# Optimization experiments

Hardware: AMD Instinct MI355X
Metric: run time of the kernel (lower is better)

## Reference

```python
import jax, jax.numpy as jnp
import numpy as np

B, T, N, C = 32, 16, 1000, 16   # batch, seq_len, num_nodes, in_channels
G, H, O = 32, 512, 8            # gcn_hidden, lstm_hidden, output_dim
E_RAND = 8000                   # random edges; + N self loops -> E = 9000


def setup_inputs() -> dict:
    key = jax.random.key(0)
    ks = jax.random.split(key, 13)
    rng = np.random.default_rng(0)
    src = rng.integers(0, N, E_RAND)
    dst = rng.integers(0, N, E_RAND)
    loop = np.arange(N)
    edge_index = jnp.asarray(
        np.stack([np.concatenate([src, loop]), np.concatenate([dst, loop])]),
        dtype=jnp.int32)
    ew = np.concatenate([rng.uniform(0.5, 1.5, E_RAND), np.ones(N)]).astype(np.float32)

    def p(k, s, sc):
        return jax.random.normal(k, s, jnp.float32) * sc

    return {
        'x': p(ks[0], (B, T, N, C), 1.0),
        'edge_index': edge_index,
        'edge_weight': jnp.asarray(ew),
        'gcn_w': p(ks[1], (T, C, G), 0.1),
        'gcn_b': p(ks[2], (T, G), 0.02),
        'w_ih0': p(ks[3], (4 * H, N * G), 0.02),
        'w_hh0': p(ks[4], (4 * H, H), 0.02),
        'b_ih0': p(ks[5], (4 * H,), 0.02),
        'b_hh0': p(ks[6], (4 * H,), 0.02),
        'w_ih1': p(ks[7], (4 * H, H), 0.02),
        'w_hh1': p(ks[8], (4 * H, H), 0.02),
        'b_ih1': p(ks[9], (4 * H,), 0.02),
        'b_hh1': p(ks[10], (4 * H,), 0.02),
        'proj_w': p(ks[11], (O, H), 0.04),
        'proj_b': p(ks[12], (O,), 0.02),
    }


def _lstm_layer(inp, w_ih, w_hh, b_ih, b_hh):
    # inp: [B, T, D]; torch gate order i, f, g, o
    pre = jnp.einsum('btd,gd->btg', inp, w_ih) + b_ih + b_hh  # [B, T, 4H]
    h0 = jnp.zeros((inp.shape[0], w_hh.shape[1]), inp.dtype)

    def step(carry, x_t):
        h, c = carry
        gates = x_t + h @ w_hh.T
        i, f, g, o = jnp.split(gates, 4, axis=-1)
        c = jax.nn.sigmoid(f) * c + jax.nn.sigmoid(i) * jnp.tanh(g)
        h = jax.nn.sigmoid(o) * jnp.tanh(c)
        return (h, c), h

    _, hs = jax.lax.scan(step, (h0, h0), pre.transpose(1, 0, 2))  # [T, B, H]
    return hs.transpose(1, 0, 2)


def reference(x, edge_index, edge_weight, gcn_w, gcn_b,
              w_ih0, w_hh0, b_ih0, b_hh0,
              w_ih1, w_hh1, b_ih1, b_hh1, proj_w, proj_b):
    src, dst = edge_index[0], edge_index[1]
    # GCN symmetric normalization (self-loops already present in edge list)
    deg = jax.ops.segment_sum(edge_weight, dst, num_segments=N)
    dinv = jnp.where(deg > 0, jax.lax.rsqrt(jnp.maximum(deg, 1e-12)), 0.0)
    norm = dinv[src] * edge_weight * dinv[dst]  # [E]
    # per-timestep linear transform: distinct GCN weight per t
    xw = jnp.einsum('btni,tio->btno', x, gcn_w)  # [B, T, N, G]
    # gather from source nodes, scale, scatter-add into targets
    msg = xw[:, :, src, :] * norm[None, None, :, None]      # [B, T, E, G]
    agg = jnp.zeros_like(xw).at[:, :, dst, :].add(msg)      # [B, T, N, G]
    h = jax.nn.relu(agg + gcn_b[None, :, None, :])
    seq = h.reshape(B, T, N * G)                            # [B, T, N*G]
    out1 = _lstm_layer(seq, w_ih0, w_hh0, b_ih0, b_hh0)
    out2 = _lstm_layer(out1, w_ih1, w_hh1, b_ih1, b_hh1)
    last = out2[:, -1, :]                                   # [B, H]
    return last @ proj_w.T + proj_b                         # [B, O]
```

## Files before the change

### kernel.cpp

```cpp
#include <hip/hip_runtime.h>
#include <hip/hip_bf16.h>

typedef unsigned short u16;
typedef __bf16 bf16x8 __attribute__((ext_vector_type(8)));
typedef float f32x4 __attribute__((ext_vector_type(4)));
typedef unsigned short u16x8 __attribute__((ext_vector_type(8)));
typedef unsigned long long u64;

#define NB 32
#define NT 16
#define NN 1000
#define NC 16
#define NG 32
#define NH 512
#define NK 32000
#define BH (NB*NH)
#define LWG 64
#define LTH 384
#define NSPLIT 8

__device__ __forceinline__ u16 f2bf(float f) {
    unsigned int u = __float_as_uint(f);
    unsigned int r = u + 0x7FFFu + ((u >> 16) & 1u);
    return (u16)(r >> 16);
}

__device__ __forceinline__ unsigned cvt2(float a, float b) {
    unsigned r;
    asm("v_cvt_pk_bf16_f32 %0, %1, %2" : "=v"(r) : "v"(a), "v"(b));
    return r;
}

__device__ __forceinline__ float sigmoidf(float x) { return 1.f / (1.f + __expf(-x)); }

__device__ __forceinline__ float dot4(float4 a, float4 b) {
    return a.x * b.x + a.y * b.y + a.z * b.z + a.w * b.w;
}

#define AT_LOAD(p)    __hip_atomic_load((p), __ATOMIC_RELAXED, __HIP_MEMORY_SCOPE_AGENT)
#define AT_STORE(p,v) __hip_atomic_store((p), (v), __ATOMIC_RELAXED, __HIP_MEMORY_SCOPE_AGENT)

#define GLOAD16(g, l) __builtin_amdgcn_global_load_lds( \
    (const __attribute__((address_space(1))) void*)(g),  \
    (__attribute__((address_space(3))) void*)(l), 16, 0, 0)

__global__ void graph_prep(const int* __restrict__ ei, const float* __restrict__ ew, int E,
                           int* __restrict__ rowptr, int* __restrict__ csr_src,
                           float* __restrict__ csr_nrm) {
    __shared__ float degs[NN];
    __shared__ float dinv[NN];
    __shared__ int cnt[NN];
    __shared__ int rp[NN + 1];
    __shared__ int wsum[16];
    int tid = threadIdx.x, lane = tid & 63, wid = tid >> 6;
    for (int n = tid; n < NN; n += 1024) { degs[n] = 0.f; cnt[n] = 0; }
    __syncthreads();
    for (int e = tid; e < E; e += 1024) {
        int d = ei[E + e];
        atomicAdd(&degs[d], ew[e]);
        atomicAdd(&cnt[d], 1);
    }
    __syncthreads();
    for (int n = tid; n < NN; n += 1024) {
        float d = degs[n];
        dinv[n] = d > 0.f ? rsqrtf(fmaxf(d, 1e-12f)) : 0.f;
    }
    int v = (tid < NN) ? cnt[tid] : 0;
    int inc = v;
#pragma unroll
    for (int d = 1; d < 64; d <<= 1) {
        int u = __shfl_up(inc, d, 64);
        if (lane >= d) inc += u;
    }
    if (lane == 63) wsum[wid] = inc;
    __syncthreads();
    if (tid == 0) {
        int a = 0;
#pragma unroll
        for (int i = 0; i < 16; ++i) { int t = wsum[i]; wsum[i] = a; a += t; }
    }
    __syncthreads();
    int excl = inc - v + wsum[wid];
    if (tid <= NN) { rp[tid] = excl; rowptr[tid] = excl; }
    if (tid < NN) cnt[tid] = 0;
    __syncthreads();
    for (int e = tid; e < E; e += 1024) {
        int d = ei[E + e], s = ei[e];
        int pos = rp[d] + atomicAdd(&cnt[d], 1);
        csr_src[pos] = s;
        csr_nrm[pos] = dinv[s] * ew[e] * dinv[d];
    }
}

__global__ __launch_bounds__(1024) void gcn_fused(const float* __restrict__ x,
                                                  const float* __restrict__ gw,
                                                  const float* __restrict__ gb,
                                                  const int* __restrict__ rowptr,
                                                  const int* __restrict__ csr_src,
                                                  const float* __restrict__ csr_nrm,
                                                  u16* __restrict__ seq) {
    __shared__ float xwlds[NN * NG];
    __shared__ float wlds[NC * NG];
    __shared__ int rplds[NN + 1];
    int bt = blockIdx.x;
    int t = bt & 15;
    int tid = threadIdx.x;
    int g = tid & 31, grp = tid >> 5;

    for (int i = tid; i < NC * NG; i += 1024) wlds[i] = gw[t * NC * NG + i];
    for (int i = tid; i <= NN; i += 1024) rplds[i] = rowptr[i];
    __syncthreads();

    const float* xbt = x + (size_t)bt * NN * NC;
    for (int r = grp; r < NN; r += 32) {
        const float4* xr = (const float4*)(xbt + r * NC);
        float4 a0 = xr[0], a1 = xr[1], a2 = xr[2], a3 = xr[3];
        float acc = a0.x * wlds[g]        + a0.y * wlds[32 + g]
                  + a0.z * wlds[64 + g]   + a0.w * wlds[96 + g]
                  + a1.x * wlds[128 + g]  + a1.y * wlds[160 + g]
                  + a1.z * wlds[192 + g]  + a1.w * wlds[224 + g]
                  + a2.x * wlds[256 + g]  + a2.y * wlds[288 + g]
                  + a2.z * wlds[320 + g]  + a2.w * wlds[352 + g]
                  + a3.x * wlds[384 + g]  + a3.y * wlds[416 + g]
                  + a3.z * wlds[448 + g]  + a3.w * wlds[480 + g];
        xwlds[r * NG + g] = acc;
    }
    __syncthreads();

    float bias = gb[t * NG + g];
    u16* seqbt = seq + (size_t)bt * NK;
    for (int n = grp; n < NN; n += 32) {
        int p0 = rplds[n], p1 = rplds[n + 1];
        float acc = 0.f;
        for (int p = p0; p < p1; ++p)
            acc += csr_nrm[p] * xwlds[csr_src[p] * NG + g];
        seqbt[n * NG + g] = f2bf(fmaxf(acc + bias, 0.f));
    }
}

__global__ __launch_bounds__(256) void gemm_f32b(const u16* __restrict__ A,
                                                 const float* __restrict__ Bw,
                                                 float* __restrict__ part) {
    __shared__ __align__(16) u16 As[2][128 * 64];
    __shared__ __align__(16) u16 Bs[2][128 * 64];
    int tid = threadIdx.x;
    int lane = tid & 63, wid = tid >> 6;
    int wr = wid >> 1, wc = wid & 1;
    int bid = blockIdx.x;
    int s = bid & 7;
    int idx = bid >> 3;
    int tm = (idx & 3) * 128, tn = (idx >> 2) * 128;
    int ks0 = s * 62 + (s < 4 ? s : 4);
    int ksn = (s < 4) ? 63 : 62;

    int srow = tid >> 3, sc = tid & 7;
    int sce = sc ^ (srow & 7);
    const u16* gaBase = A + (size_t)(tm + srow) * NK + (size_t)ks0 * 64 + sce * 8;
    int br = tid >> 3, bc = tid & 7;
    int bce = bc ^ (br & 7);
    const float* gbBase = Bw + (size_t)(tn + br) * NK + (size_t)ks0 * 64 + bce * 8;

    f32x4 acc[4][4];
#pragma unroll
    for (int i = 0; i < 4; ++i)
#pragma unroll
        for (int j = 0; j < 4; ++j) acc[i][j] = (f32x4){0.f, 0.f, 0.f, 0.f};

    int fr = lane & 15, kq = lane >> 4, fs = fr & 7;

    float4 bqA[8], bqB[8];

    auto issueA = [&](int kt, int buf) {
#pragma unroll
        for (int q = 0; q < 4; ++q)
            GLOAD16(gaBase + (size_t)kt * 64 + (size_t)q * 32 * NK,
                    &As[buf][0] + srow * 64 + sc * 8 + q * 32 * 64);
    };
    auto loadB = [&](int kt, float4* dst) {
        const float* g = gbBase + (size_t)kt * 64;
#pragma unroll
        for (int q = 0; q < 4; ++q) {
            dst[2 * q]     = *(const float4*)(g + (size_t)q * 32 * NK);
            dst[2 * q + 1] = *(const float4*)(g + (size_t)q * 32 * NK + 4);
        }
    };
    auto cvtB = [&](const float4* src, int buf) {
#pragma unroll
        for (int q = 0; q < 4; ++q) {
            uint4 w;
            w.x = cvt2(src[2 * q].x, src[2 * q].y);
            w.y = cvt2(src[2 * q].z, src[2 * q].w);
            w.z = cvt2(src[2 * q + 1].x, src[2 * q + 1].y);
            w.w = cvt2(src[2 * q + 1].z, src[2 * q + 1].w);
            *(uint4*)(&Bs[buf][0] + (br + q * 32) * 64 + bc * 8) = w;
        }
    };
    auto mfmaStep = [&](int buf) {
        const u16* Ap = &As[buf][0];
        const u16* Bp = &Bs[buf][0];
#pragma unroll
        for (int kk = 0; kk < 2; ++kk) {
            int c0 = ((kq + kk * 4) ^ fs) * 8;
            bf16x8 af[4], bv[4];
#pragma unroll
            for (int fm = 0; fm < 4; ++fm)
                af[fm] = *(const bf16x8*)(Ap + (wr * 64 + fm * 16 + fr) * 64 + c0);
#pragma unroll
            for (int fn = 0; fn < 4; ++fn)
                bv[fn] = *(const bf16x8*)(Bp + (wc * 64 + fn * 16 + fr) * 64 + c0);
#pragma unroll
            for (int fm = 0; fm < 4; ++fm)
#pragma unroll
                for (int fn = 0; fn < 4; ++fn)
                    acc[fm][fn] = __builtin_amdgcn_mfma_f32_16x16x32_bf16(af[fm], bv[fn], acc[fm][fn], 0, 0, 0);
        }
    };

    issueA(0, 0);
    loadB(0, bqA);
    loadB(ksn > 1 ? 1 : 0, bqB);
    cvtB(bqA, 0);
    asm volatile("s_waitcnt lgkmcnt(0)" ::: "memory");
    asm volatile("s_barrier" ::: "memory");

#define STEP(KS, P, CUR, NXT)                                                  \
    {                                                                          \
        int kA = (KS) + 1 < ksn ? (KS) + 1 : ksn - 1;                          \
        int kB = (KS) + 2 < ksn ? (KS) + 2 : ksn - 1;                          \
        issueA(kA, (P) ^ 1);                         \
        loadB(kB, NXT);                     \
        mfmaStep(P);                                                           \
        cvtB(CUR, (P) ^ 1);                    \
        asm volatile("s_waitcnt vmcnt(8) lgkmcnt(0)" ::: "memory");            \
        asm volatile("s_barrier" ::: "memory");                                \
    }

    int ks = 0;
    while (ks + 2 <= ksn) {
        STEP(ks, 0, bqB, bqA);
        STEP(ks + 1, 1, bqA, bqB);
        ks += 2;
    }
    if (ks < ksn) {
        STEP(ks, 0, bqB, bqA);
    }
#undef STEP

    int rq = lane >> 4;
    size_t base = (size_t)s * 512 * 2048;
#pragma unroll
    for (int fm = 0; fm < 4; ++fm)
#pragma unroll
        for (int fn = 0; fn < 4; ++fn)
#pragma unroll
            for (int rr = 0; rr < 4; ++rr) {
                int m = tm + wr * 64 + fm * 16 + rq * 4 + rr;
                int n = tn + wc * 64 + fn * 16 + (lane & 15);
                part[base + (size_t)m * 2048 + n] = acc[fm][fn][rr];
            }
}

__global__ __launch_bounds__(256) void reduce_bias_p(const float* __restrict__ part,
                                                     const float* __restrict__ b_ih0,
                                                     const float* __restrict__ b_hh0,
                                                     float* __restrict__ pre0p) {
    int s = blockIdx.y;
    int r = blockIdx.x * 64 + (threadIdx.x & 63);
    int bq = threadIdx.x >> 6;
    float bias = b_ih0[r] + b_hh0[r];
#pragma unroll
    for (int b8 = 0; b8 < 8; ++b8) {
        int b = bq * 8 + b8;
        float acc = bias;
#pragma unroll
        for (int sk = 0; sk < NSPLIT; ++sk)
            acc += part[(size_t)sk * 1048576 + (size_t)(b * 16 + s) * 2048 + r];
        pre0p[((size_t)s * 2048 + r) * 32 + b] = acc;
    }
}

__global__ __launch_bounds__(256) void wperm(const float* __restrict__ w_hh0,
                                             const float* __restrict__ w_ih1,
                                             const float* __restrict__ w_hh1,
                                             u16* __restrict__ Wbig) {
    int rt = blockIdx.x;
    int wg = blockIdx.y;
    int tid = threadIdx.x;
#pragma unroll
    for (int it = 0; it < 4; ++it) {
        int idx = it * 256 + tid;
        int kt = idx >> 6, lane = idx & 63;
        int p = rt * 16 + (lane & 15);
        int gate = (p & 31) >> 3;
        int col = wg * 8 + (p & 7);
        const float* src;
        if (p < 32)      src = w_hh0 + (size_t)(gate * NH + col) * NH;
        else if (p < 64) src = w_ih1 + (size_t)(gate * NH + col) * NH;
        else             src = w_hh1 + (size_t)(gate * NH + col) * NH;
        int k0 = kt * 32 + (lane >> 4) * 8;
        float4 v0 = *(const float4*)(src + k0);
        float4 v1 = *(const float4*)(src + k0 + 4);
        u16x8 o;
        o[0] = f2bf(v0.x); o[1] = f2bf(v0.y); o[2] = f2bf(v0.z); o[3] = f2bf(v0.w);
        o[4] = f2bf(v1.x); o[5] = f2bf(v1.y); o[6] = f2bf(v1.z); o[7] = f2bf(v1.w);
        *(u16x8*)(Wbig + (((size_t)wg * 6 + rt) * 16 + kt) * 512 + lane * 8) = o;
    }
}

__global__ void init2(u16* h0, u16* h1, int* flags) {
    int i = blockIdx.x * 256 + threadIdx.x;
    if (i < 2 * BH) { h0[i] = 0; h1[i] = 0; }
    if (i < 1024) flags[i] = 0;
}

__global__ __launch_bounds__(LTH) void lstm2(const u16* __restrict__ Wbig,
                                             const float* __restrict__ pre0p,
                                             const float* __restrict__ b_ih1,
                                             const float* __restrict__ b_hh1,
                                             u16* __restrict__ h0buf,
                                             u16* __restrict__ h1buf,
                                             float* __restrict__ h1f,
                                             int* __restrict__ flags) {
    __shared__ __align__(16) u16 hA0[32 * 520];
    __shared__ __align__(16) u16 hA1[32 * 520];
    __shared__ float G[96][33];
    __shared__ float cst[2][8][32];
    __shared__ u16 hst[2][8][32];
    int wg = blockIdx.x, tid = threadIdx.x;
    int wid = tid >> 6, lane = tid & 63;
    int grp = wid >> 1;

    bf16x8 af[16];
    const u16* wsrc = Wbig + (size_t)wg * 49152 + wid * 8192 + lane * 8;
#pragma unroll
    for (int kt = 0; kt < 16; ++kt) af[kt] = *(const bf16x8*)(wsrc + kt * 512);

    if (tid < 512) ((float*)cst)[tid] = 0.f;

    int uj = (tid >> 5) & 7, ub = tid & 31;
    int ucol = wg * 8 + uj;
    float bs0 = 0.f, bs1 = 0.f, bs2 = 0.f, bs3 = 0.f;
    if (tid < 256) {
        bs0 = b_ih1[ucol] + b_hh1[ucol];
        bs1 = b_ih1[NH + ucol] + b_hh1[NH + ucol];
        bs2 = b_ih1[2 * NH + ucol] + b_hh1[2 * NH + ucol];
        bs3 = b_ih1[3 * NH + ucol] + b_hh1[3 * NH + ucol];
    }
    __syncthreads();

    for (int s = 0; s <= 16; ++s) {
        for (int r = wid; r < 64; r += 6) {
            const u64* src = (r < 32)
                ? (const u64*)(h0buf + ((s & 1) ^ 1) * BH + r * 512)
                : (const u64*)(h1buf + (s & 1) * BH + (r - 32) * 512);
            u16* dst = (r < 32) ? (hA0 + r * 520) : (hA1 + (r - 32) * 520);
            u64 v0 = AT_LOAD(src + lane);
            u64 v1 = AT_LOAD(src + 64 + lane);
            *(u64*)(dst + lane * 4) = v0;
            *(u64*)(dst + 256 + lane * 4) = v1;
        }
        float up0 = 0.f, up1 = 0.f, up2 = 0.f, up3 = 0.f;
        if (tid < 256 && s < 16) {
            const float* pp = pre0p + (size_t)s * 2048 * 32 + ub;
            up0 = pp[(size_t)ucol * 32];
            up1 = pp[((size_t)NH + ucol) * 32];
            up2 = pp[((size_t)2 * NH + ucol) * 32];
            up3 = pp[((size_t)3 * NH + ucol) * 32];
        }
        __syncthreads();

        bool active = (grp == 0) ? (s < 16) : (s >= 1);
        if (active) {
            const u16* hA = (grp < 2) ? hA0 : hA1;
            const u16* hp = hA + (lane & 15) * 520 + (lane >> 4) * 8;
            f32x4 a0 = (f32x4){0.f, 0.f, 0.f, 0.f};
            f32x4 a1 = (f32x4){0.f, 0.f, 0.f, 0.f};
#pragma unroll
            for (int kt = 0; kt < 16; ++kt) {
                bf16x8 b0 = *(const bf16x8*)(hp + kt * 32);
                bf16x8 b1 = *(const bf16x8*)(hp + 16 * 520 + kt * 32);
                a0 = __builtin_amdgcn_mfma_f32_16x16x32_bf16(af[kt], b0, a0, 0, 0, 0);
                a1 = __builtin_amdgcn_mfma_f32_16x16x32_bf16(af[kt], b1, a1, 0, 0, 0);
            }
            int r0 = wid * 16 + (lane >> 4) * 4;
#pragma unroll
            for (int rr = 0; rr < 4; ++rr) {
                G[r0 + rr][lane & 15] = a0[rr];
                G[r0 + rr][16 + (lane & 15)] = a1[rr];
            }
        }
        __syncthreads();

        if (tid < 256) {
            if (s < 16) {
                float gi = G[uj][ub] + up0;
                float gf = G[8 + uj][ub] + up1;
                float gg = G[16 + uj][ub] + up2;
                float go = G[24 + uj][ub] + up3;
                float c = sigmoidf(gf) * cst[0][uj][ub] + sigmoidf(gi) * tanhf(gg);
                cst[0][uj][ub] = c;
                hst[0][uj][ub] = f2bf(sigmoidf(go) * tanhf(c));
            }
            if (s >= 1) {
                float gi = G[32 + uj][ub] + G[64 + uj][ub] + bs0;
                float gf = G[40 + uj][ub] + G[72 + uj][ub] + bs1;
                float gg = G[48 + uj][ub] + G[80 + uj][ub] + bs2;
                float go = G[56 + uj][ub] + G[88 + uj][ub] + bs3;
                float c = sigmoidf(gf) * cst[1][uj][ub] + sigmoidf(gi) * tanhf(gg);
                cst[1][uj][ub] = c;
                float hv = sigmoidf(go) * tanhf(c);
                hst[1][uj][ub] = f2bf(hv);
                if (s == 16) h1f[ub * NH + ucol] = hv;
            }
        }
        __syncthreads();

        if (s < 16) {
            if (wid == 0) {
                if (lane < 32) {
                    union { u16 a[8]; u64 q[2]; } v;
#pragma unroll
                    for (int j = 0; j < 8; ++j) v.a[j] = hst[0][j][lane];
                    u64* d = (u64*)(h0buf + (s & 1) * BH + lane * 512 + wg * 8);
                    AT_STORE(d, v.q[0]); AT_STORE(d + 1, v.q[1]);
                } else if (s >= 1) {
                    int b = lane - 32;
                    union { u16 a[8]; u64 q[2]; } v;
#pragma unroll
                    for (int j = 0; j < 8; ++j) v.a[j] = hst[1][j][b];
                    u64* d = (u64*)(h1buf + ((s - 1) & 1) * BH + b * 512 + wg * 8);
                    AT_STORE(d, v.q[0]); AT_STORE(d + 1, v.q[1]);
                }
                asm volatile("s_waitcnt vmcnt(0)" ::: "memory");
                if (lane == 0) AT_STORE(&flags[wg * 16], s + 1);
                int target = s + 1;
                for (;;) {
                    int v = AT_LOAD(&flags[lane * 16]);
                    if (__all(v >= target)) break;
                    __builtin_amdgcn_s_sleep(1);
                }
            }
            __syncthreads();
        }
    }
}

__global__ __launch_bounds__(1024) void proj_k(const float* __restrict__ h1f,
                                               const float* __restrict__ proj_w,
                                               const float* __restrict__ proj_b,
                                               float* __restrict__ out) {
    __shared__ float pj[32][8][4];
    int tid = threadIdx.x;
    int b = tid >> 5, o = (tid >> 2) & 7, kq = tid & 3;
    const float4* hp = (const float4*)(h1f + (size_t)b * NH + kq * 128);
    const float4* wp = (const float4*)(proj_w + (size_t)o * NH + kq * 128);
    float acc = 0.f;
#pragma unroll 8
    for (int k = 0; k < 32; ++k) acc += dot4(hp[k], wp[k]);
    pj[b][o][kq] = acc;
    __syncthreads();
    if (tid < 256) {
        int bb = tid >> 3, oo = tid & 7;
        out[bb * 8 + oo] = pj[bb][oo][0] + pj[bb][oo][1] + pj[bb][oo][2] + pj[bb][oo][3] + proj_b[oo];
    }
}

extern "C" void kernel_launch(void* const* d_in, const int* in_sizes, int n_in,
                              void* d_out, int out_size, void* d_ws, size_t ws_size,
                              hipStream_t stream) {
    const float* x      = (const float*)d_in[0];
    const int*   ei     = (const int*)d_in[1];
    const float* ew     = (const float*)d_in[2];
    const float* gcn_w  = (const float*)d_in[3];
    const float* gcn_b  = (const float*)d_in[4];
    const float* w_ih0  = (const float*)d_in[5];
    const float* w_hh0  = (const float*)d_in[6];
    const float* b_ih0  = (const float*)d_in[7];
    const float* b_hh0  = (const float*)d_in[8];
    const float* w_ih1  = (const float*)d_in[9];
    const float* w_hh1  = (const float*)d_in[10];
    const float* b_ih1  = (const float*)d_in[11];
    const float* b_hh1  = (const float*)d_in[12];
    const float* proj_w = (const float*)d_in[13];
    const float* proj_b = (const float*)d_in[14];
    int E = in_sizes[2];

    char* ws = (char*)d_ws;
    size_t off = 0;
    float* part   = (float*)(ws + off);
    u16* Wbig     = (u16*)part;        off += 50331648;
    u16* seq      = (u16*)(ws + off);  off += 32768000;
    float* pre0p  = (float*)(ws + off); off += 4194304;
    u16* h0buf    = (u16*)(ws + off);  off += 2 * BH * 2;
    u16* h1buf    = (u16*)(ws + off);  off += 2 * BH * 2;
    float* h1f    = (float*)(ws + off); off += BH * 4;
    int* flags    = (int*)(ws + off);  off += 4096;
    int* rowptr   = (int*)(ws + off);  off += 4096;
    int* csr_src  = (int*)(ws + off);  off += 36864;
    float* csr_nrm = (float*)(ws + off); off += 36864;
    (void)ws_size; (void)n_in; (void)out_size;

    graph_prep<<<1, 1024, 0, stream>>>(ei, ew, E, rowptr, csr_src, csr_nrm);
    gcn_fused<<<512, 1024, 0, stream>>>(x, gcn_w, gcn_b, rowptr, csr_src, csr_nrm, seq);
    gemm_f32b<<<512, 256, 0, stream>>>(seq, w_ih0, part);
    reduce_bias_p<<<dim3(32, 16), 256, 0, stream>>>(part, b_ih0, b_hh0, pre0p);
    wperm<<<dim3(6, 64), 256, 0, stream>>>(w_hh0, w_ih1, w_hh1, Wbig);
    init2<<<128, 256, 0, stream>>>(h0buf, h1buf, flags);

    lstm2<<<LWG, LTH, 0, stream>>>(Wbig, pre0p, b_ih1, b_hh1, h0buf, h1buf, h1f, flags);
    proj_k<<<1, 1024, 0, stream>>>(h1f, proj_w, proj_b, (float*)d_out);
}
```

Baseline: 444.0 us.

## Restructure split-K input GEMM to load A directly into registers with 512x64 tiles

The layer-0 input-projection GEMM now covers all 512 rows per block with an N-tile of 64 (8 waves of 64 rows each). The A operand (bf16 GCN output) is read from global memory straight into MFMA register fragments instead of being staged through LDS; only the fp32 weight tile is converted and put in shared memory. This halves the grid to 256 blocks of 512 threads and removes the A LDS traffic and its async copies. In exchange, each fp32 weight element is read from HBM only once, but the A loads are strided 16-byte accesses per lane with less coalescing, and there is less explicit vmcnt-based overlap.

```diff
diff --git a/kernel.cpp b/kernel.cpp
--- a/kernel.cpp
+++ b/kernel.cpp
@@ -138,27 +138,27 @@
     }
 }
 
-__global__ __launch_bounds__(256) void gemm_f32b(const u16* __restrict__ A,
-                                                 const float* __restrict__ Bw,
-                                                 float* __restrict__ part) {
-    __shared__ __align__(16) u16 As[2][128 * 64];
-    __shared__ __align__(16) u16 Bs[2][128 * 64];
+__global__ __launch_bounds__(512) void gemm_sk(const u16* __restrict__ A,
+                                               const float* __restrict__ Bw,
+                                               float* __restrict__ part) {
+    __shared__ __align__(16) u16 Bs[2][64 * 64];
     int tid = threadIdx.x;
-    int lane = tid & 63, wid = tid >> 6;
-    int wr = wid >> 1, wc = wid & 1;
+    int lane = tid & 63, w = tid >> 6;
     int bid = blockIdx.x;
     int s = bid & 7;
-    int idx = bid >> 3;
-    int tm = (idx & 3) * 128, tn = (idx >> 2) * 128;
+    int tn = (bid >> 3) * 64;
     int ks0 = s * 62 + (s < 4 ? s : 4);
     int ksn = (s < 4) ? 63 : 62;
-
-    int srow = tid >> 3, sc = tid & 7;
-    int sce = sc ^ (srow & 7);
-    const u16* gaBase = A + (size_t)(tm + srow) * NK + (size_t)ks0 * 64 + sce * 8;
+    int fr = lane & 15, kq = lane >> 4, fs = fr & 7;
+
+    const u16* aRow0 = A + (size_t)(w * 64 +  0 + fr) * NK + (size_t)ks0 * 64 + kq * 8;
+    const u16* aRow1 = A + (size_t)(w * 64 + 16 + fr) * NK + (size_t)ks0 * 64 + kq * 8;
+    const u16* aRow2 = A + (size_t)(w * 64 + 32 + fr) * NK + (size_t)ks0 * 64 + kq * 8;
+    const u16* aRow3 = A + (size_t)(w * 64 + 48 + fr) * NK + (size_t)ks0 * 64 + kq * 8;
+
     int br = tid >> 3, bc = tid & 7;
-    int bce = bc ^ (br & 7);
-    const float* gbBase = Bw + (size_t)(tn + br) * NK + (size_t)ks0 * 64 + bce * 8;
+    const float* gB = Bw + (size_t)(tn + br) * NK + (size_t)ks0 * 64 + bc * 8;
+    int bwr = br * 64 + (bc ^ (br & 7)) * 8;
 
     f32x4 acc[4][4];
 #pragma unroll
@@ -166,85 +166,74 @@
 #pragma unroll
         for (int j = 0; j < 4; ++j) acc[i][j] = (f32x4){0.f, 0.f, 0.f, 0.f};
 
-    int fr = lane & 15, kq = lane >> 4, fs = fr & 7;
-
-    float4 bqA[8], bqB[8];
-
-    auto issueA = [&](int kt, int buf) {
-#pragma unroll
-        for (int q = 0; q < 4; ++q)
-            GLOAD16(gaBase + (size_t)kt * 64 + (size_t)q * 32 * NK,
-                    &As[buf][0] + srow * 64 + sc * 8 + q * 32 * 64);
+    bf16x8 aA[8], aB[8];
+    float4 bA[2], bB[2];
+
+    auto loadA = [&](int ks, bf16x8* dst) {
+        size_t o = (size_t)ks * 64;
+        dst[0] = *(const bf16x8*)(aRow0 + o);      dst[1] = *(const bf16x8*)(aRow0 + o + 32);
+        dst[2] = *(const bf16x8*)(aRow1 + o);      dst[3] = *(const bf16x8*)(aRow1 + o + 32);
+        dst[4] = *(const bf16x8*)(aRow2 + o);      dst[5] = *(const bf16x8*)(aRow2 + o + 32);
+        dst[6] = *(const bf16x8*)(aRow3 + o);      dst[7] = *(const bf16x8*)(aRow3 + o + 32);
     };
-    auto loadB = [&](int kt, float4* dst) {
-        const float* g = gbBase + (size_t)kt * 64;
-#pragma unroll
-        for (int q = 0; q < 4; ++q) {
-            dst[2 * q]     = *(const float4*)(g + (size_t)q * 32 * NK);
-            dst[2 * q + 1] = *(const float4*)(g + (size_t)q * 32 * NK + 4);
+    auto loadBf = [&](int ks, float4* dst) {
+        const float* g = gB + (size_t)ks * 64;
+        dst[0] = *(const float4*)g;
+        dst[1] = *(const float4*)(g + 4);
+    };
+    auto cvtWriteB = [&](const float4* src, int p) {
+        uint4 v;
+        v.x = cvt2(src[0].x, src[0].y); v.y = cvt2(src[0].z, src[0].w);
+        v.z = cvt2(src[1].x, src[1].y); v.w = cvt2(src[1].z, src[1].w);
+        *(uint4*)(&Bs[p][0] + bwr) = v;
+    };
+    auto mfmaStep = [&](const bf16x8* ar, int p) {
+#pragma unroll
+        for (int kk = 0; kk < 2; ++kk) {
+            bf16x8 bv[4];
+#pragma unroll
+            for (int fn = 0; fn < 4; ++fn) {
+                int row = fn * 16 + fr;
+                int chunk = (kq + kk * 4) ^ fs;
+                bv[fn] = *(const bf16x8*)(&Bs[p][0] + row * 64 + chunk * 8);
+            }
+#pragma unroll
+            for (int fm = 0; fm < 4; ++fm)
+#pragma unroll
+                for (int fn = 0; fn < 4; ++fn)
+                    acc[fm][fn] = __builtin_amdgcn_mfma_f32_16x16x32_bf16(ar[fm * 2 + kk], bv[fn], acc[fm][fn], 0, 0, 0);
         }
     };
-    auto cvtB = [&](const float4* src, int buf) {
-#pragma unroll
-        for (int q = 0; q < 4; ++q) {
-            uint4 w;
-            w.x = cvt2(src[2 * q].x, src[2 * q].y);
-            w.y = cvt2(src[2 * q].z, src[2 * q].w);
-            w.z = cvt2(src[2 * q + 1].x, src[2 * q + 1].y);
-            w.w = cvt2(src[2 * q + 1].z, src[2 * q + 1].w);
-            *(uint4*)(&Bs[buf][0] + (br + q * 32) * 64 + bc * 8) = w;
-        }
-    };
-    auto mfmaStep = [&](int buf) {
-        const u16* Ap = &As[buf][0];
-        const u16* Bp = &Bs[buf][0];
-#pragma unroll
-        for (int kk = 0; kk < 2; ++kk) {
-            int c0 = ((kq + kk * 4) ^ fs) * 8;
-            bf16x8 af[4], bv[4];
-#pragma unroll
-            for (int fm = 0; fm < 4; ++fm)
-                af[fm] = *(const bf16x8*)(Ap + (wr * 64 + fm * 16 + fr) * 64 + c0);
-#pragma unroll
-            for (int fn = 0; fn < 4; ++fn)
-                bv[fn] = *(const bf16x8*)(Bp + (wc * 64 + fn * 16 + fr) * 64 + c0);
-#pragma unroll
-            for (int fm = 0; fm < 4; ++fm)
-#pragma unroll
-                for (int fn = 0; fn < 4; ++fn)
-                    acc[fm][fn] = __builtin_amdgcn_mfma_f32_16x16x32_bf16(af[fm], bv[fn], acc[fm][fn], 0, 0, 0);
-        }
-    };
-
-    issueA(0, 0);
-    loadB(0, bqA);
-    loadB(ksn > 1 ? 1 : 0, bqB);
-    cvtB(bqA, 0);
+
+    loadA(0, aA);
+    loadBf(0, bA);
+    loadBf(ksn > 1 ? 1 : 0, bB);
+    cvtWriteB(bA, 0);
     asm volatile("s_waitcnt lgkmcnt(0)" ::: "memory");
     asm volatile("s_barrier" ::: "memory");
 
-#define STEP(KS, P, CUR, NXT)                                                  \
+#define GSTEP(KS, P, CA, NA, CB, NB_)                                          \
     {                                                                          \
         int kA = (KS) + 1 < ksn ? (KS) + 1 : ksn - 1;                          \
         int kB = (KS) + 2 < ksn ? (KS) + 2 : ksn - 1;                          \
-        issueA(kA, (P) ^ 1);                         \
-        loadB(kB, NXT);                     \
-        mfmaStep(P);                                                           \
-        cvtB(CUR, (P) ^ 1);                    \
-        asm volatile("s_waitcnt vmcnt(8) lgkmcnt(0)" ::: "memory");            \
+        loadA(kA, NA);                                                         \
+        loadBf(kB, NB_);                                                       \
+        mfmaStep(CA, P);                                                       \
+        cvtWriteB(CB, (P) ^ 1);                                                \
+        asm volatile("s_waitcnt lgkmcnt(0)" ::: "memory");                     \
         asm volatile("s_barrier" ::: "memory");                                \
     }
 
     int ks = 0;
     while (ks + 2 <= ksn) {
-        STEP(ks, 0, bqB, bqA);
-        STEP(ks + 1, 1, bqA, bqB);
+        GSTEP(ks, 0, aA, aB, bB, bA);
+        GSTEP(ks + 1, 1, aB, aA, bA, bB);
         ks += 2;
     }
     if (ks < ksn) {
-        STEP(ks, 0, bqB, bqA);
-    }
-#undef STEP
+        GSTEP(ks, 0, aA, aB, bB, bA);
+    }
+#undef GSTEP
 
     int rq = lane >> 4;
     size_t base = (size_t)s * 512 * 2048;
@@ -254,8 +243,8 @@
         for (int fn = 0; fn < 4; ++fn)
 #pragma unroll
             for (int rr = 0; rr < 4; ++rr) {
-                int m = tm + wr * 64 + fm * 16 + rq * 4 + rr;
-                int n = tn + wc * 64 + fn * 16 + (lane & 15);
+                int m = w * 64 + fm * 16 + rq * 4 + rr;
+                int n = tn + fn * 16 + (lane & 15);
                 part[base + (size_t)m * 2048 + n] = acc[fm][fn][rr];
             }
 }
@@ -502,7 +491,7 @@
 
     graph_prep<<<1, 1024, 0, stream>>>(ei, ew, E, rowptr, csr_src, csr_nrm);
     gcn_fused<<<512, 1024, 0, stream>>>(x, gcn_w, gcn_b, rowptr, csr_src, csr_nrm, seq);
-    gemm_f32b<<<512, 256, 0, stream>>>(seq, w_ih0, part);
+    gemm_sk<<<256, 512, 0, stream>>>(seq, w_ih0, part);
     reduce_bias_p<<<dim3(32, 16), 256, 0, stream>>>(part, b_ih0, b_hh0, pre0p);
     wperm<<<dim3(6, 64), 256, 0, stream>>>(w_hh0, w_ih1, w_hh1, Wbig);
     init2<<<128, 256, 0, stream>>>(h0buf, h1buf, flags);
```

Result: slower. 470.8 us (+6.0%).

## Double split-K, single-buffer LDS GEMM with nontemporal weight loads

Applied to the files above, without the earlier changes.

Raises the split-K factor of the big input-projection GEMM from 8 to 16 and launches 1024 blocks instead of 512, halving the K range per block for more parallelism. LDS drops from double to single buffer, which should allow more resident blocks per CU, and the B tile load is reorganised so each thread reads contiguous 32-float runs. Weight loads, partial stores and the reduce loads become nontemporal to avoid polluting cache. The cost is twice as much partial-sum traffic and reduce work, a larger workspace, and an extra barrier per step that removes load/compute overlap within a block.

```diff
diff --git a/kernel.cpp b/kernel.cpp
--- a/kernel.cpp
+++ b/kernel.cpp
@@ -4,6 +4,7 @@
 typedef unsigned short u16;
 typedef __bf16 bf16x8 __attribute__((ext_vector_type(8)));
 typedef float f32x4 __attribute__((ext_vector_type(4)));
+typedef float f32x4v __attribute__((ext_vector_type(4)));
 typedef unsigned short u16x8 __attribute__((ext_vector_type(8)));
 typedef unsigned long long u64;
 
@@ -17,7 +18,7 @@
 #define BH (NB*NH)
 #define LWG 64
 #define LTH 384
-#define NSPLIT 8
+#define NSPLIT 16
 
 __device__ __forceinline__ u16 f2bf(float f) {
     unsigned int u = __float_as_uint(f);
@@ -138,27 +139,28 @@
     }
 }
 
-__global__ __launch_bounds__(256) void gemm_f32b(const u16* __restrict__ A,
+__global__ __launch_bounds__(256) void gemm_f32c(const u16* __restrict__ A,
                                                  const float* __restrict__ Bw,
                                                  float* __restrict__ part) {
-    __shared__ __align__(16) u16 As[2][128 * 64];
-    __shared__ __align__(16) u16 Bs[2][128 * 64];
+    __shared__ __align__(16) u16 As[128 * 64];
+    __shared__ __align__(16) u16 Bs[128 * 64];
     int tid = threadIdx.x;
     int lane = tid & 63, wid = tid >> 6;
     int wr = wid >> 1, wc = wid & 1;
     int bid = blockIdx.x;
-    int s = bid & 7;
-    int idx = bid >> 3;
+    int s = bid & 15;
+    int idx = bid >> 4;
     int tm = (idx & 3) * 128, tn = (idx >> 2) * 128;
-    int ks0 = s * 62 + (s < 4 ? s : 4);
-    int ksn = (s < 4) ? 63 : 62;
+    int ks0 = s * 31 + (s < 4 ? s : 4);
+    int ksn = (s < 4) ? 32 : 31;
 
     int srow = tid >> 3, sc = tid & 7;
     int sce = sc ^ (srow & 7);
     const u16* gaBase = A + (size_t)(tm + srow) * NK + (size_t)ks0 * 64 + sce * 8;
-    int br = tid >> 3, bc = tid & 7;
-    int bce = bc ^ (br & 7);
-    const float* gbBase = Bw + (size_t)(tn + br) * NK + (size_t)ks0 * 64 + bce * 8;
+    u16* la = As + srow * 64 + sc * 8;
+
+    int br = tid >> 1, bh = tid & 1;
+    const float* gbBase = Bw + (size_t)(tn + br) * NK + (size_t)ks0 * 64 + bh * 32;
 
     f32x4 acc[4][4];
 #pragma unroll
@@ -168,46 +170,44 @@
 
     int fr = lane & 15, kq = lane >> 4, fs = fr & 7;
 
-    float4 bqA[8], bqB[8];
-
-    auto issueA = [&](int kt, int buf) {
+    f32x4v bqA[8], bqB[8];
+
+    auto issueA = [&](int ks) {
 #pragma unroll
         for (int q = 0; q < 4; ++q)
-            GLOAD16(gaBase + (size_t)kt * 64 + (size_t)q * 32 * NK,
-                    &As[buf][0] + srow * 64 + sc * 8 + q * 32 * 64);
+            GLOAD16(gaBase + (size_t)ks * 64 + (size_t)q * 32 * NK, la + q * 32 * 64);
     };
-    auto loadB = [&](int kt, float4* dst) {
-        const float* g = gbBase + (size_t)kt * 64;
-#pragma unroll
-        for (int q = 0; q < 4; ++q) {
-            dst[2 * q]     = *(const float4*)(g + (size_t)q * 32 * NK);
-            dst[2 * q + 1] = *(const float4*)(g + (size_t)q * 32 * NK + 4);
+    auto loadBf = [&](int ks, f32x4v* d) {
+        const float* g = gbBase + (size_t)ks * 64;
+#pragma unroll
+        for (int j = 0; j < 4; ++j) {
+            d[2 * j]     = __builtin_nontemporal_load((const f32x4v*)(g + j * 8));
+            d[2 * j + 1] = __builtin_nontemporal_load((const f32x4v*)(g + j * 8 + 4));
         }
     };
-    auto cvtB = [&](const float4* src, int buf) {
-#pragma unroll
-        for (int q = 0; q < 4; ++q) {
-            uint4 w;
-            w.x = cvt2(src[2 * q].x, src[2 * q].y);
-            w.y = cvt2(src[2 * q].z, src[2 * q].w);
-            w.z = cvt2(src[2 * q + 1].x, src[2 * q + 1].y);
-            w.w = cvt2(src[2 * q + 1].z, src[2 * q + 1].w);
-            *(uint4*)(&Bs[buf][0] + (br + q * 32) * 64 + bc * 8) = w;
+    auto cvtWriteB = [&](const f32x4v* src) {
+#pragma unroll
+        for (int j = 0; j < 4; ++j) {
+            uint4 v;
+            v.x = cvt2(src[2 * j][0], src[2 * j][1]);
+            v.y = cvt2(src[2 * j][2], src[2 * j][3]);
+            v.z = cvt2(src[2 * j + 1][0], src[2 * j + 1][1]);
+            v.w = cvt2(src[2 * j + 1][2], src[2 * j + 1][3]);
+            int cphys = (bh * 4 + j) ^ (br & 7);
+            *(uint4*)(Bs + br * 64 + cphys * 8) = v;
         }
     };
-    auto mfmaStep = [&](int buf) {
-        const u16* Ap = &As[buf][0];
-        const u16* Bp = &Bs[buf][0];
+    auto mfmaStep = [&]() {
 #pragma unroll
         for (int kk = 0; kk < 2; ++kk) {
             int c0 = ((kq + kk * 4) ^ fs) * 8;
             bf16x8 af[4], bv[4];
 #pragma unroll
             for (int fm = 0; fm < 4; ++fm)
-                af[fm] = *(const bf16x8*)(Ap + (wr * 64 + fm * 16 + fr) * 64 + c0);
+                af[fm] = *(const bf16x8*)(As + (wr * 64 + fm * 16 + fr) * 64 + c0);
 #pragma unroll
             for (int fn = 0; fn < 4; ++fn)
-                bv[fn] = *(const bf16x8*)(Bp + (wc * 64 + fn * 16 + fr) * 64 + c0);
+                bv[fn] = *(const bf16x8*)(Bs + (wc * 64 + fn * 16 + fr) * 64 + c0);
 #pragma unroll
             for (int fm = 0; fm < 4; ++fm)
 #pragma unroll
@@ -216,35 +216,31 @@
         }
     };
 
-    issueA(0, 0);
-    loadB(0, bqA);
-    loadB(ksn > 1 ? 1 : 0, bqB);
-    cvtB(bqA, 0);
-    asm volatile("s_waitcnt lgkmcnt(0)" ::: "memory");
-    asm volatile("s_barrier" ::: "memory");
-
-#define STEP(KS, P, CUR, NXT)                                                  \
+    loadBf(0, bqA);
+
+#define FSTEP(KS, CUR, NXT)                                                    \
     {                                                                          \
-        int kA = (KS) + 1 < ksn ? (KS) + 1 : ksn - 1;                          \
-        int kB = (KS) + 2 < ksn ? (KS) + 2 : ksn - 1;                          \
-        issueA(kA, (P) ^ 1);                         \
-        loadB(kB, NXT);                     \
-        mfmaStep(P);                                                           \
-        cvtB(CUR, (P) ^ 1);                    \
+        asm volatile("s_barrier" ::: "memory");              \
+        issueA(KS);                                                            \
+        __builtin_amdgcn_sched_barrier(0);                 \
+        int kB = (KS) + 1 < ksn ? (KS) + 1 : ksn - 1;                          \
+        loadBf(kB, NXT);                                                       \
+        cvtWriteB(CUR);                                                        \
         asm volatile("s_waitcnt vmcnt(8) lgkmcnt(0)" ::: "memory");            \
         asm volatile("s_barrier" ::: "memory");                                \
+        mfmaStep();                                                            \
     }
 
     int ks = 0;
     while (ks + 2 <= ksn) {
-        STEP(ks, 0, bqB, bqA);
-        STEP(ks + 1, 1, bqA, bqB);
+        FSTEP(ks, bqA, bqB);
+        FSTEP(ks + 1, bqB, bqA);
         ks += 2;
     }
     if (ks < ksn) {
-        STEP(ks, 0, bqB, bqA);
-    }
-#undef STEP
+        FSTEP(ks, bqA, bqB);
+    }
+#undef FSTEP
 
     int rq = lane >> 4;
     size_t base = (size_t)s * 512 * 2048;
@@ -256,7 +252,8 @@
             for (int rr = 0; rr < 4; ++rr) {
                 int m = tm + wr * 64 + fm * 16 + rq * 4 + rr;
                 int n = tn + wc * 64 + fn * 16 + (lane & 15);
-                part[base + (size_t)m * 2048 + n] = acc[fm][fn][rr];
+                __builtin_nontemporal_store(acc[fm][fn][rr],
+                                            &part[base + (size_t)m * 2048 + n]);
             }
 }
 
@@ -274,7 +271,8 @@
         float acc = bias;
 #pragma unroll
         for (int sk = 0; sk < NSPLIT; ++sk)
-            acc += part[(size_t)sk * 1048576 + (size_t)(b * 16 + s) * 2048 + r];
+            acc += __builtin_nontemporal_load(
+                &part[(size_t)sk * 1048576 + (size_t)(b * 16 + s) * 2048 + r]);
         pre0p[((size_t)s * 2048 + r) * 32 + b] = acc;
     }
 }
@@ -488,7 +486,7 @@
     char* ws = (char*)d_ws;
     size_t off = 0;
     float* part   = (float*)(ws + off);
-    u16* Wbig     = (u16*)part;        off += 50331648;
+    u16* Wbig     = (u16*)part;        off += 67108864;
     u16* seq      = (u16*)(ws + off);  off += 32768000;
     float* pre0p  = (float*)(ws + off); off += 4194304;
     u16* h0buf    = (u16*)(ws + off);  off += 2 * BH * 2;
@@ -502,7 +500,7 @@
 
     graph_prep<<<1, 1024, 0, stream>>>(ei, ew, E, rowptr, csr_src, csr_nrm);
     gcn_fused<<<512, 1024, 0, stream>>>(x, gcn_w, gcn_b, rowptr, csr_src, csr_nrm, seq);
-    gemm_f32b<<<512, 256, 0, stream>>>(seq, w_ih0, part);
+    gemm_f32c<<<1024, 256, 0, stream>>>(seq, w_ih0, part);
     reduce_bias_p<<<dim3(32, 16), 256, 0, stream>>>(part, b_ih0, b_hh0, pre0p);
     wperm<<<dim3(6, 64), 256, 0, stream>>>(w_hh0, w_ih1, w_hh1, Wbig);
     init2<<<128, 256, 0, stream>>>(h0buf, h1buf, flags);
```

After: 812.0 us. 1.83x slower.
